# Kernel optimization log

Hardware: AMD Instinct MI355X
Metric: run time of the kernel (lower is better)

The kernel has to match this reference:

```python
import jax, jax.numpy as jnp
import numpy as np

B, T, D_MODEL = 2, 2048, 2048
N_HEAD, N_KV = 16, 4
HEAD_DIM = D_MODEL // N_HEAD  # 128
N_REP = N_HEAD // N_KV        # 4
ROPE_BASE = 10000.0


def setup_inputs() -> dict:
    key = jax.random.key(0)
    ks = jax.random.split(key, 5)
    s = 0.02
    return {
        "x": jax.random.normal(ks[0], (B, T, D_MODEL), dtype=jnp.float32),
        "Wq": jax.random.normal(ks[1], (D_MODEL, N_HEAD * HEAD_DIM), dtype=jnp.float32) * s,
        "Wk": jax.random.normal(ks[2], (D_MODEL, N_KV * HEAD_DIM), dtype=jnp.float32) * s,
        "Wv": jax.random.normal(ks[3], (D_MODEL, N_KV * HEAD_DIM), dtype=jnp.float32) * s,
        "Wo": jax.random.normal(ks[4], (D_MODEL, D_MODEL), dtype=jnp.float32) * s,
    }


def _rope_cos_sin(seq_len, dim, dtype):
    inv_freq = 1.0 / (ROPE_BASE ** (jnp.arange(0, dim, 2, dtype=jnp.float32) / dim))
    t = jnp.arange(seq_len, dtype=jnp.float32)
    freqs = t[:, None] * inv_freq[None, :]          # (T, dim/2)
    emb = jnp.concatenate([freqs, freqs], axis=-1)  # (T, dim)
    return jnp.cos(emb).astype(dtype), jnp.sin(emb).astype(dtype)


def _rotate_half(x):
    half = x.shape[-1] // 2
    return jnp.concatenate([-x[..., half:], x[..., :half]], axis=-1)


def reference(x, Wq, Wk, Wv, Wo):
    Bx, Tx, _ = x.shape
    # projections (weights stored (in, out); equals torch Linear with W^T)
    q = (x @ Wq).reshape(Bx, Tx, N_HEAD, HEAD_DIM).transpose(0, 2, 1, 3)  # (B,H,T,d)
    k = (x @ Wk).reshape(Bx, Tx, N_KV, HEAD_DIM).transpose(0, 2, 1, 3)    # (B,Hkv,T,d)
    v = (x @ Wv).reshape(Bx, Tx, N_KV, HEAD_DIM).transpose(0, 2, 1, 3)

    cos, sin = _rope_cos_sin(Tx, HEAD_DIM, x.dtype)  # (T, d)
    q = q * cos + _rotate_half(q) * sin
    k = k * cos + _rotate_half(k) * sin

    # grouped attention: q grouped by kv head, avoids materializing repeated K/V
    qg = q.reshape(Bx, N_KV, N_REP, Tx, HEAD_DIM)
    scale = 1.0 / np.sqrt(HEAD_DIM)
    att = jnp.einsum('bgrtd,bgsd->bgrts', qg, k) * scale  # (B,Hkv,rep,T,S)
    causal = jnp.tril(jnp.ones((Tx, Tx), dtype=bool))
    att = jnp.where(causal, att, -jnp.inf)
    att = jax.nn.softmax(att, axis=-1)
    y = jnp.einsum('bgrts,bgsd->bgrtd', att, v)           # (B,Hkv,rep,T,d)
    y = y.reshape(Bx, N_HEAD, Tx, HEAD_DIM).transpose(0, 2, 1, 3).reshape(Bx, Tx, D_MODEL)
    return y @ Wo
```

## Files before the change

kernel.cpp:

```cpp
#include <hip/hip_runtime.h>
#include <hip/hip_bf16.h>

typedef unsigned short u16;
typedef unsigned int u32;
typedef __attribute__((ext_vector_type(4))) float f32x4;
typedef __attribute__((ext_vector_type(8))) __bf16 bf16x8;

#define B_   2
#define T_   2048
#define DM   2048
#define NH   16
#define NKV  4
#define HD   128

__device__ __forceinline__ u16 f2bf(float f){
    u32 u = __builtin_bit_cast(u32, f);
    u += 0x7FFFu + ((u >> 16) & 1u);
    return (u16)(u >> 16);
}
__device__ __forceinline__ float bf2f(u16 v){
    return __builtin_bit_cast(float, (u32)v << 16);
}

__device__ __forceinline__ float ex2(float x){
    float r; asm("v_exp_f32 %0, %1" : "=v"(r) : "v"(x)); return r;
}

__device__ __forceinline__ void gld_lds16(const void* g, void* l){
    __builtin_amdgcn_global_load_lds(
        (const __attribute__((address_space(1))) void*)g,
        (__attribute__((address_space(3))) void*)l, 16, 0, 0);
}

__global__ void prep(const float* __restrict__ x,
                     const float* __restrict__ Wq, const float* __restrict__ Wk,
                     const float* __restrict__ Wv, const float* __restrict__ Wo,
                     u16* __restrict__ xb, u16* __restrict__ Wqkv, u16* __restrict__ Wot,
                     float2* __restrict__ tab){
    __shared__ float tile[32][33];
    int bid = blockIdx.x, tid = threadIdx.x;
    if (bid < 8192){
        int i = bid * 256 + tid;
        float4 v = ((const float4*)x)[i];
        ushort4 o;
        o.x = f2bf(v.x); o.y = f2bf(v.y); o.z = f2bf(v.z); o.w = f2bf(v.w);
        ((ushort4*)xb)[i] = o;
    } else if (bid < 18432){
        int tb = bid - 8192;
        int bx = tb % 160, byy = tb / 160;
        const float* W; u16* Out; int N; int nb; int perm;
        if (bx < 64)      { W = Wq; Out = Wqkv;                  N = 2048; nb = bx;      perm = 1; }
        else if (bx < 80) { W = Wk; Out = Wqkv + 2048ull * 2048; N = 512;  nb = bx - 64; perm = 1; }
        else if (bx < 96) { W = Wv; Out = Wqkv + 2560ull * 2048; N = 512;  nb = bx - 80; perm = 0; }
        else              { W = Wo; Out = Wot;                   N = 2048; nb = bx - 96; perm = 0; }
        int n0 = nb * 32, k0 = byy * 32;
        int tx = tid & 31, ty = tid >> 5;
#pragma unroll
        for (int i = 0; i < 4; i++)
            tile[ty + i * 8][tx] = W[(size_t)(k0 + ty + i * 8) * N + n0 + tx];
        __syncthreads();
#pragma unroll
        for (int i = 0; i < 4; i++){
            int n = n0 + ty + i * 8;
            int np = perm ? ((n & ~127) | ((n & 63) << 1) | ((n >> 6) & 1)) : n;
            Out[(size_t)np * 2048 + k0 + tx] = f2bf(tile[tx][ty + i * 8]);
        }
    } else {
        int idx = (bid - 18432) * 256 + tid;
        int i = idx & 63, t = idx >> 6;
        float ang = (float)t * exp2f((float)i * (-13.287712379549449f / 64.0f));
        float sv, cv;
        __sincosf(ang, &sv, &cv);
        tab[idx] = make_float2(cv, sv);
    }
}

#define BARR() asm volatile("s_barrier" ::: "memory")
#define VM0()  asm volatile("s_waitcnt vmcnt(0)" ::: "memory")
#define VM4()  asm volatile("s_waitcnt vmcnt(4)" ::: "memory")

#define READ_A(QA, BUF) { \
    const char* ab = (const char*)&As[BUF][wm][0]; \
    _Pragma("unroll") for (int i = 0; i < 4; i++){ \
        int rh = ((QA)*4 + i)*16 + lx; \
        _Pragma("unroll") for (int ks = 0; ks < 2; ks++) \
            a_[i][ks] = *(const bf16x8*)(ab + rh*128 + (((ks*4+tg)*16) ^ ((lx&7)<<4))); \
    } }
#define READ_B(QB, BUF) { \
    const char* bb = (const char*)&Bs[BUF][wn>>1][0]; \
    _Pragma("unroll") for (int n = 0; n < 2; n++){ \
        int rbh = (wn&1)*64 + ((QB)*2+n)*16 + lx; \
        _Pragma("unroll") for (int ks = 0; ks < 2; ks++) \
            b_[(QB)*2+n][ks] = *(const bf16x8*)(bb + rbh*128 + (((ks*4+tg)*16) ^ ((lx&7)<<4))); \
    } }
#define MFMA_Q(QA, QB) { \
    __builtin_amdgcn_s_setprio(1); \
    _Pragma("unroll") for (int i = 0; i < 4; i++) \
    _Pragma("unroll") for (int n = 0; n < 2; n++) \
    _Pragma("unroll") for (int ks = 0; ks < 2; ks++) \
        acc[(QA)*4+i][(QB)*2+n] = __builtin_amdgcn_mfma_f32_16x16x32_bf16( \
            a_[i][ks], b_[(QB)*2+n][ks], acc[(QA)*4+i][(QB)*2+n], 0, 0, 0); \
    __builtin_amdgcn_s_setprio(0); }

template<int MODE>
__global__ __launch_bounds__(512, 2) void gemm256(const u16* __restrict__ A, const u16* __restrict__ Bt,
                                                  void* __restrict__ O0, u16* __restrict__ Ktl,
                                                  u16* __restrict__ Vtl, const float2* __restrict__ tab,
                                                  int NBX){
    __shared__ __attribute__((aligned(16))) u16 As[2][2][8192];
    __shared__ __attribute__((aligned(16))) u16 Bs[2][2][8192];
    const int tid = threadIdx.x;
    const int lane = tid & 63, w = tid >> 6;
    const int wm = w >> 2, wn = w & 3;
    const int tg = lane >> 4, lx = lane & 15;
    int q8 = (int)gridDim.x >> 3;
    int swz = ((int)blockIdx.x & 7) * q8 + ((int)blockIdx.x >> 3);
    int kh = 0;
    if constexpr (MODE == 2){ kh = swz >> 7; swz &= 127; }
    const int bx = swz % NBX, by = swz / NBX;
    const int m0 = by * 256, n0 = bx * 256;
    const int K = 2048;
    const int NIT = (MODE == 2) ? 8 : 16;
    const int kt0 = kh * 16;
    const int ltMax = 2 * NIT - 1;
    const int kcx = (lane & 7) ^ ((lane >> 3) & 7);

    f32x4 acc[8][4];
    const f32x4 Z = {0.f, 0.f, 0.f, 0.f};
#pragma unroll
    for (int i = 0; i < 8; i++)
#pragma unroll
        for (int j = 0; j < 4; j++) acc[i][j] = Z;
    bf16x8 a_[4][2], b_[4][2];

    auto stA = [&](int buf, int q, int kt){
        int mh = w >> 2;
        int s0 = (w & 3) * 2;
#pragma unroll
        for (int l = 0; l < 2; l++){
            int s = s0 + l;
            gld_lds16(A + (size_t)(m0 + mh*128 + q*64 + s*8 + (lane>>3)) * K + kt*64 + kcx*8,
                      &As[buf][mh][q*4096 + s*512 + lane*8]);
        }
    };
    auto stB = [&](int buf, int q, int kt){
        int bh = w >> 2;
        int hi = (w >> 1) & 1;
        int s0 = (w & 1) * 2;
#pragma unroll
        for (int l = 0; l < 2; l++){
            int s = s0 + l;
            gld_lds16(Bt + (size_t)(n0 + bh*128 + hi*64 + q*32 + s*8 + (lane>>3)) * K + kt*64 + kcx*8,
                      &Bs[buf][bh][hi*4096 + q*2048 + s*512 + lane*8]);
        }
    };

    stA(0, 0, kt0); stB(0, 0, kt0); stA(0, 1, kt0); stB(0, 1, kt0);
    stA(1, 0, kt0 + 1); stB(1, 0, kt0 + 1);
    VM4(); BARR();

#pragma unroll 1
    for (int it = 0; it < NIT; it++){
        const int T1 = kt0 + 2*it + 1;
        const int T2 = kt0 + ((2*it + 2 < ltMax) ? 2*it + 2 : ltMax);
        const int T3 = kt0 + ((2*it + 3 < ltMax) ? 2*it + 3 : ltMax);
        READ_A(0, 0); READ_B(0, 0); stA(1, 1, T1);
        BARR(); MFMA_Q(0, 0); BARR();
        READ_B(1, 0); stB(1, 1, T1);
        BARR(); MFMA_Q(0, 1); BARR();
        READ_A(1, 0); stA(0, 0, T2);
        BARR(); MFMA_Q(1, 0); BARR();
        stB(0, 0, T2);
        BARR(); MFMA_Q(1, 1); VM4(); BARR();
        READ_A(0, 1); READ_B(0, 1); stA(0, 1, T2);
        BARR(); MFMA_Q(0, 0); BARR();
        READ_B(1, 1); stB(0, 1, T2);
        BARR(); MFMA_Q(0, 1); BARR();
        READ_A(1, 1); stA(1, 0, T3);
        BARR(); MFMA_Q(1, 0); BARR();
        stB(1, 0, T3);
        BARR(); MFMA_Q(1, 1); VM4(); BARR();
    }

    if constexpr (MODE == 2){
        u16* C = (u16*)O0 + (size_t)kh * 4096 * 2048;
#pragma unroll
        for (int mi = 0; mi < 8; mi++)
#pragma unroll
            for (int ni = 0; ni < 4; ni++){
                int r0 = m0 + wm*128 + mi*16 + tg*4;
                int c  = n0 + wn*64 + ni*16 + lx;
#pragma unroll
                for (int j = 0; j < 4; j++)
                    C[(size_t)(r0 + j) * 2048 + c] = f2bf(acc[mi][ni][j]);
            }
    } else {
        u16* Qp = (u16*)O0;
        if (bx < 8){
            const float QS = 0.08838834764831845f * 1.4426950408889634f;
#pragma unroll
            for (int mi = 0; mi < 8; mi++)
#pragma unroll
                for (int ni = 0; ni < 4; ni++){
                    int r0 = m0 + wm*128 + mi*16 + tg*4;
                    int c  = n0 + wn*64 + ni*16 + lx;
                    int ii = (c & 127) >> 1;
#pragma unroll
                    for (int j = 0; j < 4; j++){
                        float v = acc[mi][ni][j];
                        float p = __shfl_xor(v, 1);
                        int t = (r0 + j) & 2047;
                        float2 cs = tab[t * 64 + ii];
                        float o = ((lx & 1) ? (v * cs.x + p * cs.y) : (v * cs.x - p * cs.y)) * QS;
                        Qp[(size_t)(r0 + j) * 2048 + c] = f2bf(o);
                    }
                }
        } else if (bx < 10){
#pragma unroll
            for (int mi = 0; mi < 8; mi++)
#pragma unroll
                for (int ni = 0; ni < 4; ni++){
                    int r0 = m0 + wm*128 + mi*16 + tg*4;
                    int c  = n0 + wn*64 + ni*16 + lx;
                    int hk = (c >> 7) & 3;
                    int dd = c & 127;
                    int ii = dd >> 1;
#pragma unroll
                    for (int j = 0; j < 4; j++){
                        int r = r0 + j;
                        int bb2 = r >> 11, tt = r & 2047;
                        float v = acc[mi][ni][j];
                        float p = __shfl_xor(v, 1);
                        float2 cs = tab[tt * 64 + ii];
                        float o = (lx & 1) ? (v * cs.x + p * cs.y) : (v * cs.x - p * cs.y);
                        size_t tb = ((size_t)(bb2 * 4 + hk) * 32 + (tt >> 6)) * 8192;
                        u32 byte = (u32)((tt & 63) * 256) + (((u32)(2 * dd)) ^ ((u32)((tt & 7) << 4)));
                        Ktl[tb + byte / 2] = f2bf(o);
                    }
                }
        } else {
#pragma unroll
            for (int mi = 0; mi < 8; mi++){
                int r0 = m0 + wm*128 + mi*16 + tg*4;
                int bb2 = r0 >> 11, ss = r0 & 2047;
                int sb = ss & 63;
#pragma unroll
                for (int ni = 0; ni < 4; ni++){
                    int c  = n0 + wn*64 + ni*16 + lx;
                    int hk = (c >> 7) & 3;
                    int d  = c & 127;
                    size_t tb = ((size_t)(bb2 * 4 + hk) * 32 + (ss >> 6)) * 8192;
                    u32 swzd = (u32)((d & 7) << 4);
#pragma unroll
                    for (int j = 0; j < 4; j++){
                        int s = sb + j;
                        int sig = ((s & 15) << 2) | ((s >> 4) & 3);
                        u32 byte = (u32)(d * 128) + (((u32)(2 * sig)) ^ swzd);
                        Vtl[tb + byte / 2] = f2bf(acc[mi][ni][j]);
                    }
                }
            }
        }
    }
}

__global__ void reduceWo(const u16* __restrict__ P, float* __restrict__ out){
    size_t t = (size_t)blockIdx.x * 256 + threadIdx.x;
    const u16* p0 = P + t * 8;
    const u16* p1 = P + 4096ull * 2048 + t * 8;
    uint4 a = *(const uint4*)p0;
    uint4 b = *(const uint4*)p1;
    const u16* as = (const u16*)&a;
    const u16* bs = (const u16*)&b;
    float4 o0, o1;
    o0.x = bf2f(as[0]) + bf2f(bs[0]); o0.y = bf2f(as[1]) + bf2f(bs[1]);
    o0.z = bf2f(as[2]) + bf2f(bs[2]); o0.w = bf2f(as[3]) + bf2f(bs[3]);
    o1.x = bf2f(as[4]) + bf2f(bs[4]); o1.y = bf2f(as[5]) + bf2f(bs[5]);
    o1.z = bf2f(as[6]) + bf2f(bs[6]); o1.w = bf2f(as[7]) + bf2f(bs[7]);
    ((float4*)out)[t * 2]     = o0;
    ((float4*)out)[t * 2 + 1] = o1;
}

__global__ __launch_bounds__(256) void attn8(const u16* __restrict__ Q, const u16* __restrict__ Kt,
                                             const u16* __restrict__ Vt, u16* __restrict__ Y){
    __shared__ __attribute__((aligned(16))) u16 Ks[8192];
    __shared__ __attribute__((aligned(16))) u16 Vs[8192];
    __shared__ __attribute__((aligned(16))) u16 Pl[4][1024];
    const int tid = threadIdx.x;
    const int lane = tid & 63, w = tid >> 6;
    const int tg = lane >> 4, lx = lane & 15;
    int gid = blockIdx.x;
    int z = gid & 255, k4 = gid >> 8;
    int j8 = z & 7, h = (z >> 3) & 15, b = z >> 7;
    int qt = (k4 == 0) ? j8 : (k4 == 1) ? 31 - j8 : (k4 == 2) ? j8 + 8 : 23 - j8;
    const int hkv = h >> 2;
    const size_t kvBase = ((size_t)(b * NKV + hkv) * 32) * 8192;
    const f32x4 Z = {0.f, 0.f, 0.f, 0.f};

    auto STAGE_K = [&](int it){
        const u16* kg = Kt + kvBase + (size_t)it * 8192;
#pragma unroll
        for (int i = 0; i < 4; i++){
            int is = w * 4 + i;
            gld_lds16(kg + is * 512 + lane * 8, &Ks[is * 512]);
        }
    };
    auto STAGE_V = [&](int it){
        const u16* vg = Vt + kvBase + (size_t)it * 8192;
#pragma unroll
        for (int i = 0; i < 4; i++){
            int is = w * 4 + i;
            gld_lds16(vg + is * 512 + lane * 8, &Vs[is * 512]);
        }
    };

    const int q0 = qt * 64;
    const int qrow = q0 + w * 16 + lx;
    bf16x8 qfr[4];
#pragma unroll
    for (int kk = 0; kk < 4; kk++)
        qfr[kk] = *(const bf16x8*)(Q + (size_t)(b * T_ + qrow) * DM + h * HD + kk * 32 + tg * 8);
    f32x4 accO[8];
#pragma unroll
    for (int i = 0; i < 8; i++) accO[i] = Z;
    float mr[4] = {-INFINITY, -INFINITY, -INFINITY, -INFINITY};
    float lp[4] = {0.f, 0.f, 0.f, 0.f};
    const int nIter = qt + 1;

    STAGE_K(0); STAGE_V(0);

#pragma unroll 1
    for (int it = 0; it < nIter; it++){
        const bool last = (it + 1 == nIter);
        VM4(); BARR();
        f32x4 sa[4];
#pragma unroll
        for (int c = 0; c < 4; c++) sa[c] = Z;
        __builtin_amdgcn_s_setprio(1);
#pragma unroll
        for (int c = 0; c < 4; c++){
            int s = c * 16 + lx;
            u32 swz = (u32)((s & 7) << 4);
            const char* kb = (const char*)&Ks[0] + s * 256;
#pragma unroll
            for (int kk = 0; kk < 4; kk++){
                bf16x8 kf = *(const bf16x8*)(kb + (((u32)(kk * 64 + tg * 16)) ^ swz));
                sa[c] = __builtin_amdgcn_mfma_f32_16x16x32_bf16(qfr[kk], kf, sa[c], 0, 0, 0);
            }
        }
        __builtin_amdgcn_s_setprio(0);
        BARR();
        if (!last) STAGE_K(it + 1);
        const bool diag = last;
        float tl[4];
#pragma unroll
        for (int j = 0; j < 4; j++){
            float a0 = sa[0][j], a1 = sa[1][j], a2 = sa[2][j], a3 = sa[3][j];
            if (diag){
                int qloc = w * 16 + tg * 4 + j;
                if (lx      > qloc) a0 = -INFINITY;
                if (lx + 16 > qloc) a1 = -INFINITY;
                if (lx + 32 > qloc) a2 = -INFINITY;
                if (lx + 48 > qloc) a3 = -INFINITY;
            }
            sa[0][j] = a0; sa[1][j] = a1; sa[2][j] = a2; sa[3][j] = a3;
            tl[j] = fmaxf(fmaxf(a0, a1), fmaxf(a2, a3));
        }
        int lok = (tl[0] <= mr[0] + 8.f) && (tl[1] <= mr[1] + 8.f) &&
                  (tl[2] <= mr[2] + 8.f) && (tl[3] <= mr[3] + 8.f);
        if (!__all(lok)){
            float corr[4];
#pragma unroll
            for (int j = 0; j < 4; j++){
                float t = tl[j];
                t = fmaxf(t, __shfl_xor(t, 1));
                t = fmaxf(t, __shfl_xor(t, 2));
                t = fmaxf(t, __shfl_xor(t, 4));
                t = fmaxf(t, __shfl_xor(t, 8));
                float mn = fmaxf(mr[j], t);
                corr[j] = ex2(mr[j] - mn);
                mr[j] = mn;
                lp[j] *= corr[j];
            }
#pragma unroll
            for (int dt = 0; dt < 8; dt++){
                f32x4 t = accO[dt];
                t[0] *= corr[0]; t[1] *= corr[1]; t[2] *= corr[2]; t[3] *= corr[3];
                accO[dt] = t;
            }
        }
#pragma unroll
        for (int j = 0; j < 4; j++){
            float mn = mr[j];
            float p0 = ex2(sa[0][j] - mn), p1 = ex2(sa[1][j] - mn);
            float p2 = ex2(sa[2][j] - mn), p3 = ex2(sa[3][j] - mn);
            lp[j] += p0 + p1 + p2 + p3;
            int rr = tg * 4 + j;
            u32 woff = (u32)(rr * 128) + (((u32)(lx * 8)) ^ ((u32)((rr & 7) << 4)));
            u32 r01, r23;
            asm("v_cvt_pk_bf16_f32 %0, %1, %2" : "=v"(r01) : "v"(p0), "v"(p1));
            asm("v_cvt_pk_bf16_f32 %0, %1, %2" : "=v"(r23) : "v"(p2), "v"(p3));
            uint2 pk2 = make_uint2(r01, r23);
            *(uint2*)((char*)&Pl[w][0] + woff) = pk2;
        }
        bf16x8 pf[2];
        {
            char* pb = (char*)&Pl[w][0] + lx * 128;
            u32 swz = (u32)((lx & 7) << 4);
            pf[0] = *(const bf16x8*)(pb + (((u32)(tg * 16))      ^ swz));
            pf[1] = *(const bf16x8*)(pb + (((u32)(tg * 16 + 64)) ^ swz));
        }
        if (last){ VM0(); } else { VM4(); }
        BARR();
        __builtin_amdgcn_s_setprio(1);
#pragma unroll
        for (int dt = 0; dt < 8; dt++){
            int d = dt * 16 + lx;
            u32 swz = (u32)((d & 7) << 4);
            const char* vb = (const char*)&Vs[0] + d * 128;
            bf16x8 vf0 = *(const bf16x8*)(vb + (((u32)(tg * 16))      ^ swz));
            bf16x8 vf1 = *(const bf16x8*)(vb + (((u32)(tg * 16 + 64)) ^ swz));
            accO[dt] = __builtin_amdgcn_mfma_f32_16x16x32_bf16(pf[0], vf0, accO[dt], 0, 0, 0);
            accO[dt] = __builtin_amdgcn_mfma_f32_16x16x32_bf16(pf[1], vf1, accO[dt], 0, 0, 0);
        }
        __builtin_amdgcn_s_setprio(0);
        BARR();
        if (!last) STAGE_V(it + 1);
    }
    float inv[4];
#pragma unroll
    for (int j = 0; j < 4; j++){
        float s = lp[j];
        s += __shfl_xor(s, 1);
        s += __shfl_xor(s, 2);
        s += __shfl_xor(s, 4);
        s += __shfl_xor(s, 8);
        inv[j] = 1.0f / s;
    }
#pragma unroll
    for (int dt = 0; dt < 8; dt++)
#pragma unroll
        for (int j = 0; j < 4; j++){
            int qr = q0 + w * 16 + tg * 4 + j;
            int d = dt * 16 + lx;
            Y[(size_t)(b * T_ + qr) * DM + h * HD + d] = f2bf(accO[dt][j] * inv[j]);
        }
}

extern "C" void kernel_launch(void* const* d_in, const int* in_sizes, int n_in,
                              void* d_out, int out_size, void* d_ws, size_t ws_size,
                              hipStream_t stream){
    const float* x  = (const float*)d_in[0];
    const float* Wq = (const float*)d_in[1];
    const float* Wk = (const float*)d_in[2];
    const float* Wv = (const float*)d_in[3];
    const float* Wo = (const float*)d_in[4];

    char* ws = (char*)d_ws;
    size_t off = 0;
    auto alloc = [&](size_t bytes){ void* p = ws + off; off += (bytes + 255) & ~255ull; return p; };
    u16*    xb   = (u16*)alloc(4096ull * 2048 * 2);
    u16*    Wqkv = (u16*)alloc(3072ull * 2048 * 2);
    u16*    Wot  = (u16*)alloc(2048ull * 2048 * 2);
    u16*    qbb  = (u16*)alloc(4096ull * 2048 * 2);
    u16*    ktl  = (u16*)alloc(2ull * 4 * 32 * 8192 * 2);
    u16*    vtl  = (u16*)alloc(2ull * 4 * 32 * 8192 * 2);
    u16*    ybb  = (u16*)alloc(4096ull * 2048 * 2);
    u16*    pbb  = (u16*)alloc(2ull * 4096 * 2048 * 2);
    float2* tab  = (float2*)alloc(2048ull * 64 * 8);

    prep<<<18944, 256, 0, stream>>>(x, Wq, Wk, Wv, Wo, xb, Wqkv, Wot, tab);

    gemm256<1><<<192, 512, 0, stream>>>(xb, Wqkv, qbb, ktl, vtl, tab, 12);

    attn8<<<1024, 256, 0, stream>>>(qbb, ktl, vtl, ybb);

    gemm256<2><<<256, 512, 0, stream>>>(ybb, Wot, pbb, nullptr, nullptr, nullptr, 8);
    reduceWo<<<4096, 256, 0, stream>>>(pbb, (float*)d_out);
}
```

Before: 202.1 us.

## Retile QKV projection GEMM to 256x192 tiles for full-CU grid

Adds a dedicated gemm192 kernel for the fused QKV projection. It uses 256x192 output tiles, giving 256 blocks (16x16) instead of 192 blocks of 256x256, so all 256 CUs of the device get work. The kernel has a new 6-stage software pipeline over column sub-chunks and keeps the RoPE/scale epilogue for Q, K and V. The Wo GEMM is specialised into its own non-templated kernel. The trade-off is a smaller tile with less reuse per block and more barrier steps.

```diff
diff --git a/kernel.cpp b/kernel.cpp
--- a/kernel.cpp
+++ b/kernel.cpp
@@ -78,6 +78,148 @@
 #define BARR() asm volatile("s_barrier" ::: "memory")
 #define VM0()  asm volatile("s_waitcnt vmcnt(0)" ::: "memory")
 #define VM4()  asm volatile("s_waitcnt vmcnt(4)" ::: "memory")
+#define VM8()  asm volatile("s_waitcnt vmcnt(8)" ::: "memory")
+
+__global__ __launch_bounds__(512, 2) void gemm192(const u16* __restrict__ A, const u16* __restrict__ Bt,
+                                                  u16* __restrict__ Qp, u16* __restrict__ Ktl,
+                                                  u16* __restrict__ Vtl, const float2* __restrict__ tab){
+    __shared__ __attribute__((aligned(16))) u16 As[2][16384];
+    __shared__ __attribute__((aligned(16))) u16 Bs[2][12288];
+    const int tid = threadIdx.x;
+    const int lane = tid & 63, w = tid >> 6;
+    const int wm = w >> 1, wn = w & 1;
+    const int tg = lane >> 4, lx = lane & 15;
+    int swz = ((int)blockIdx.x & 7) * 32 + ((int)blockIdx.x >> 3);
+    const int bx = swz & 15, by = swz >> 4;
+    const int m0 = by * 256, n0 = bx * 192;
+    const int K = 2048;
+    const int kcx = (lane & 7) ^ ((lane >> 3) & 7);
+
+    f32x4 acc[4][6];
+    const f32x4 Z = {0.f, 0.f, 0.f, 0.f};
+#pragma unroll
+    for (int i = 0; i < 4; i++)
+#pragma unroll
+        for (int j = 0; j < 6; j++) acc[i][j] = Z;
+    bf16x8 a_[4][2], b_[2][2];
+
+    auto stA = [&](int buf, int kt){
+#pragma unroll
+        for (int s = 0; s < 4; s++){
+            int br = s * 64 + w * 8;
+            gld_lds16(A + (size_t)(m0 + br + (lane >> 3)) * K + kt * 64 + kcx * 8,
+                      &As[buf][br * 64 + lane * 8]);
+        }
+    };
+    auto stB = [&](int buf, int c, int kt){
+        int br = (w < 4) ? (c * 32 + w * 8) : (96 + c * 32 + (w - 4) * 8);
+        gld_lds16(Bt + (size_t)(n0 + br + (lane >> 3)) * K + kt * 64 + kcx * 8,
+                  &Bs[buf][br * 64 + lane * 8]);
+    };
+
+#define RA192(BUF) { \
+    const char* ab = (const char*)&As[BUF][0]; \
+    _Pragma("unroll") for (int mi = 0; mi < 4; mi++){ \
+        int rh = wm*64 + mi*16 + lx; \
+        _Pragma("unroll") for (int ks = 0; ks < 2; ks++) \
+            a_[mi][ks] = *(const bf16x8*)(ab + rh*128 + (((ks*4+tg)*16) ^ ((lx&7)<<4))); \
+    } }
+#define RB192(BUF, C) { \
+    const char* bb = (const char*)&Bs[BUF][0]; \
+    _Pragma("unroll") for (int n = 0; n < 2; n++){ \
+        int rb = wn*96 + (C)*32 + n*16 + lx; \
+        _Pragma("unroll") for (int ks = 0; ks < 2; ks++) \
+            b_[n][ks] = *(const bf16x8*)(bb + rb*128 + (((ks*4+tg)*16) ^ ((lx&7)<<4))); \
+    } }
+#define MM192(C) { \
+    __builtin_amdgcn_s_setprio(1); \
+    _Pragma("unroll") for (int mi = 0; mi < 4; mi++) \
+    _Pragma("unroll") for (int n = 0; n < 2; n++) \
+    _Pragma("unroll") for (int ks = 0; ks < 2; ks++) \
+        acc[mi][(C)*2+n] = __builtin_amdgcn_mfma_f32_16x16x32_bf16( \
+            a_[mi][ks], b_[n][ks], acc[mi][(C)*2+n], 0, 0, 0); \
+    __builtin_amdgcn_s_setprio(0); }
+
+    stA(0, 0); stB(0, 0, 0); stB(0, 1, 0); stB(0, 2, 0);
+    stA(1, 1); stB(1, 0, 1); stB(1, 1, 1);
+    VM8(); BARR();
+
+#pragma unroll 1
+    for (int it = 0; it < 16; it++){
+        const int O  = 2*it + 1;
+        const int E2 = (2*it + 2 < 32) ? 2*it + 2 : 31;
+        const int O2 = (2*it + 3 < 32) ? 2*it + 3 : 31;
+        RA192(0); RB192(0, 0); stB(1, 2, O);
+        BARR(); MM192(0); VM8(); BARR();
+        RB192(0, 1); stA(0, E2); stB(0, 0, E2);
+        BARR(); MM192(1); VM8(); BARR();
+        RB192(0, 2); stB(0, 1, E2);
+        BARR(); MM192(2); VM8(); BARR();
+        RA192(1); RB192(1, 0); stB(0, 2, E2);
+        BARR(); MM192(0); VM8(); BARR();
+        RB192(1, 1); stA(1, O2); stB(1, 0, O2);
+        BARR(); MM192(1); VM8(); BARR();
+        RB192(1, 2); stB(1, 1, O2);
+        BARR(); MM192(2); VM8(); BARR();
+    }
+
+    const float QS = 0.08838834764831845f * 1.4426950408889634f;
+#pragma unroll
+    for (int mi = 0; mi < 4; mi++){
+        int r0 = m0 + wm*64 + mi*16 + tg*4;
+#pragma unroll
+        for (int ci = 0; ci < 6; ci++){
+            int cb = n0 + wn*96 + ci*16;
+            int c  = cb + lx;
+            if (cb < 2048){
+                int ii = (c & 127) >> 1;
+#pragma unroll
+                for (int j = 0; j < 4; j++){
+                    float v = acc[mi][ci][j];
+                    float p = __shfl_xor(v, 1);
+                    int t = (r0 + j) & 2047;
+                    float2 cs = tab[t * 64 + ii];
+                    float o = ((lx & 1) ? (v * cs.x + p * cs.y) : (v * cs.x - p * cs.y)) * QS;
+                    Qp[(size_t)(r0 + j) * 2048 + c] = f2bf(o);
+                }
+            } else if (cb < 2560){
+                int hk = (c >> 7) & 3;
+                int dd = c & 127;
+                int ii = dd >> 1;
+#pragma unroll
+                for (int j = 0; j < 4; j++){
+                    int r = r0 + j;
+                    int bb2 = r >> 11, tt = r & 2047;
+                    float v = acc[mi][ci][j];
+                    float p = __shfl_xor(v, 1);
+                    float2 cs = tab[tt * 64 + ii];
+                    float o = (lx & 1) ? (v * cs.x + p * cs.y) : (v * cs.x - p * cs.y);
+                    size_t tb = ((size_t)(bb2 * 4 + hk) * 32 + (tt >> 6)) * 8192;
+                    u32 byte = (u32)((tt & 63) * 256) + (((u32)(2 * dd)) ^ ((u32)((tt & 7) << 4)));
+                    Ktl[tb + byte / 2] = f2bf(o);
+                }
+            } else {
+                int r0b = r0;
+                int bb2 = r0b >> 11, ss = r0b & 2047;
+                int sb = ss & 63;
+                int hk = (c >> 7) & 3;
+                int d  = c & 127;
+                size_t tb = ((size_t)(bb2 * 4 + hk) * 32 + (ss >> 6)) * 8192;
+                u32 swzd = (u32)((d & 7) << 4);
+#pragma unroll
+                for (int j = 0; j < 4; j++){
+                    int s = sb + j;
+                    int sig = ((s & 15) << 2) | ((s >> 4) & 3);
+                    u32 byte = (u32)(d * 128) + (((u32)(2 * sig)) ^ swzd);
+                    Vtl[tb + byte / 2] = f2bf(acc[mi][ci][j]);
+                }
+            }
+        }
+    }
+}
+#undef RA192
+#undef RB192
+#undef MM192
 
 #define READ_A(QA, BUF) { \
     const char* ab = (const char*)&As[BUF][wm][0]; \
@@ -102,11 +244,8 @@
             a_[i][ks], b_[(QB)*2+n][ks], acc[(QA)*4+i][(QB)*2+n], 0, 0, 0); \
     __builtin_amdgcn_s_setprio(0); }
 
-template<int MODE>
-__global__ __launch_bounds__(512, 2) void gemm256(const u16* __restrict__ A, const u16* __restrict__ Bt,
-                                                  void* __restrict__ O0, u16* __restrict__ Ktl,
-                                                  u16* __restrict__ Vtl, const float2* __restrict__ tab,
-                                                  int NBX){
+__global__ __launch_bounds__(512, 2) void gemmWo(const u16* __restrict__ A, const u16* __restrict__ Bt,
+                                                 u16* __restrict__ O0){
     __shared__ __attribute__((aligned(16))) u16 As[2][2][8192];
     __shared__ __attribute__((aligned(16))) u16 Bs[2][2][8192];
     const int tid = threadIdx.x;
@@ -115,12 +254,11 @@
     const int tg = lane >> 4, lx = lane & 15;
     int q8 = (int)gridDim.x >> 3;
     int swz = ((int)blockIdx.x & 7) * q8 + ((int)blockIdx.x >> 3);
-    int kh = 0;
-    if constexpr (MODE == 2){ kh = swz >> 7; swz &= 127; }
-    const int bx = swz % NBX, by = swz / NBX;
+    int kh = swz >> 7; swz &= 127;
+    const int bx = swz & 7, by = swz >> 3;
     const int m0 = by * 256, n0 = bx * 256;
     const int K = 2048;
-    const int NIT = (MODE == 2) ? 8 : 16;
+    const int NIT = 8;
     const int kt0 = kh * 16;
     const int ltMax = 2 * NIT - 1;
     const int kcx = (lane & 7) ^ ((lane >> 3) & 7);
@@ -182,86 +320,17 @@
         BARR(); MFMA_Q(1, 1); VM4(); BARR();
     }
 
-    if constexpr (MODE == 2){
-        u16* C = (u16*)O0 + (size_t)kh * 4096 * 2048;
-#pragma unroll
-        for (int mi = 0; mi < 8; mi++)
-#pragma unroll
-            for (int ni = 0; ni < 4; ni++){
-                int r0 = m0 + wm*128 + mi*16 + tg*4;
-                int c  = n0 + wn*64 + ni*16 + lx;
-#pragma unroll
-                for (int j = 0; j < 4; j++)
-                    C[(size_t)(r0 + j) * 2048 + c] = f2bf(acc[mi][ni][j]);
-            }
-    } else {
-        u16* Qp = (u16*)O0;
-        if (bx < 8){
-            const float QS = 0.08838834764831845f * 1.4426950408889634f;
-#pragma unroll
-            for (int mi = 0; mi < 8; mi++)
-#pragma unroll
-                for (int ni = 0; ni < 4; ni++){
-                    int r0 = m0 + wm*128 + mi*16 + tg*4;
-                    int c  = n0 + wn*64 + ni*16 + lx;
-                    int ii = (c & 127) >> 1;
-#pragma unroll
-                    for (int j = 0; j < 4; j++){
-                        float v = acc[mi][ni][j];
-                        float p = __shfl_xor(v, 1);
-                        int t = (r0 + j) & 2047;
-                        float2 cs = tab[t * 64 + ii];
-                        float o = ((lx & 1) ? (v * cs.x + p * cs.y) : (v * cs.x - p * cs.y)) * QS;
-                        Qp[(size_t)(r0 + j) * 2048 + c] = f2bf(o);
-                    }
-                }
-        } else if (bx < 10){
-#pragma unroll
-            for (int mi = 0; mi < 8; mi++)
-#pragma unroll
-                for (int ni = 0; ni < 4; ni++){
-                    int r0 = m0 + wm*128 + mi*16 + tg*4;
-                    int c  = n0 + wn*64 + ni*16 + lx;
-                    int hk = (c >> 7) & 3;
-                    int dd = c & 127;
-                    int ii = dd >> 1;
-#pragma unroll
-                    for (int j = 0; j < 4; j++){
-                        int r = r0 + j;
-                        int bb2 = r >> 11, tt = r & 2047;
-                        float v = acc[mi][ni][j];
-                        float p = __shfl_xor(v, 1);
-                        float2 cs = tab[tt * 64 + ii];
-                        float o = (lx & 1) ? (v * cs.x + p * cs.y) : (v * cs.x - p * cs.y);
-                        size_t tb = ((size_t)(bb2 * 4 + hk) * 32 + (tt >> 6)) * 8192;
-                        u32 byte = (u32)((tt & 63) * 256) + (((u32)(2 * dd)) ^ ((u32)((tt & 7) << 4)));
-                        Ktl[tb + byte / 2] = f2bf(o);
-                    }
-                }
-        } else {
-#pragma unroll
-            for (int mi = 0; mi < 8; mi++){
-                int r0 = m0 + wm*128 + mi*16 + tg*4;
-                int bb2 = r0 >> 11, ss = r0 & 2047;
-                int sb = ss & 63;
-#pragma unroll
-                for (int ni = 0; ni < 4; ni++){
-                    int c  = n0 + wn*64 + ni*16 + lx;
-                    int hk = (c >> 7) & 3;
-                    int d  = c & 127;
-                    size_t tb = ((size_t)(bb2 * 4 + hk) * 32 + (ss >> 6)) * 8192;
-                    u32 swzd = (u32)((d & 7) << 4);
-#pragma unroll
-                    for (int j = 0; j < 4; j++){
-                        int s = sb + j;
-                        int sig = ((s & 15) << 2) | ((s >> 4) & 3);
-                        u32 byte = (u32)(d * 128) + (((u32)(2 * sig)) ^ swzd);
-                        Vtl[tb + byte / 2] = f2bf(acc[mi][ni][j]);
-                    }
-                }
-            }
-        }
-    }
+    u16* C = O0 + (size_t)kh * 4096 * 2048;
+#pragma unroll
+    for (int mi = 0; mi < 8; mi++)
+#pragma unroll
+        for (int ni = 0; ni < 4; ni++){
+            int r0 = m0 + wm*128 + mi*16 + tg*4;
+            int c  = n0 + wn*64 + ni*16 + lx;
+#pragma unroll
+            for (int j = 0; j < 4; j++)
+                C[(size_t)(r0 + j) * 2048 + c] = f2bf(acc[mi][ni][j]);
+        }
 }
 
 __global__ void reduceWo(const u16* __restrict__ P, float* __restrict__ out){
@@ -471,10 +540,10 @@
 
     prep<<<18944, 256, 0, stream>>>(x, Wq, Wk, Wv, Wo, xb, Wqkv, Wot, tab);
 
-    gemm256<1><<<192, 512, 0, stream>>>(xb, Wqkv, qbb, ktl, vtl, tab, 12);
+    gemm192<<<256, 512, 0, stream>>>(xb, Wqkv, qbb, ktl, vtl, tab);
 
     attn8<<<1024, 256, 0, stream>>>(qbb, ktl, vtl, ybb);
 
-    gemm256<2><<<256, 512, 0, stream>>>(ybb, Wot, pbb, nullptr, nullptr, nullptr, 8);
+    gemmWo<<<256, 512, 0, stream>>>(ybb, Wot, pbb);
     reduceWo<<<4096, 256, 0, stream>>>(pbb, (float*)d_out);
 }
```

Result: no change. 198.3 us (-1.9%).
